# Optimization experiments

Hardware: AMD Instinct MI355X
Metric: run time of the kernel (lower is better)

## Reference

```python
import jax, jax.numpy as jnp
import numpy as np

NUM_CLASSES = 80
MAX_MATCHES = 10
ALPHA = 0.5
BETA = 6.0
EPS = 1e-9
IMG = 640.0


def _make_boxes(key, shape):
    # random valid xyxy boxes inside a 640x640 image
    k1, k2 = jax.random.split(key)
    c = jax.random.uniform(k1, shape + (2,)) * IMG
    wh = jax.random.uniform(k2, shape + (2,)) * (IMG * 0.3) + 4.0
    return jnp.concatenate([c - wh / 2, c + wh / 2], axis=-1).astype(jnp.float32)


def setup_inputs() -> dict:
    key = jax.random.key(0)
    ks = jax.random.split(key, 5)
    B, G = 32, 100
    # anchor center points for 640x640 input at strides 8/16/32 -> 8400 anchors
    pts = []
    for s in (8, 16, 32):
        n = 640 // s
        xs = (jnp.arange(n, dtype=jnp.float32) + 0.5) * s
        gy, gx = jnp.meshgrid(xs, xs, indexing="ij")
        pts.append(jnp.stack([gx.ravel(), gy.ravel()], axis=-1))
    anchors = jnp.concatenate(pts, axis=0)  # [8400, 2]
    A = anchors.shape[0]
    scores = jax.random.uniform(ks[0], (B, A, NUM_CLASSES), dtype=jnp.float32)
    decode_bboxes = _make_boxes(ks[1], (B, A))
    gt_bboxes = _make_boxes(ks[2], (B, G))
    gt_labels = jax.random.randint(ks[3], (B, G), 0, NUM_CLASSES, dtype=jnp.int32)
    gt_mask = jax.random.uniform(ks[4], (B, G)) < 0.8
    return {"scores": scores, "decode_bboxes": decode_bboxes, "anchors": anchors,
            "gt_labels": gt_labels, "gt_bboxes": gt_bboxes, "gt_mask": gt_mask}


def _pairwise_iou(gt, pred):
    # gt [B,G,4], pred [B,A,4] -> IoU [B,G,A]
    lt = jnp.maximum(gt[:, :, None, :2], pred[:, None, :, :2])
    rb = jnp.minimum(gt[:, :, None, 2:], pred[:, None, :, 2:])
    wh = jnp.clip(rb - lt, 0.0)
    inter = wh[..., 0] * wh[..., 1]
    area_g = (gt[..., 2] - gt[..., 0]) * (gt[..., 3] - gt[..., 1])
    area_p = (pred[..., 2] - pred[..., 0]) * (pred[..., 3] - pred[..., 1])
    return inter / (area_g[:, :, None] + area_p[:, None, :] - inter + EPS)


def _assign(scores, decode_bboxes, anchors, gt_labels, gt_bboxes, gt_mask):
    B, A, C = scores.shape
    G = gt_labels.shape[1]
    overlaps = _pairwise_iou(gt_bboxes, decode_bboxes)  # [B,G,A]
    # predicted score at each gt's class, per anchor -> [B,G,A]
    bbox_scores = jnp.take_along_axis(scores, gt_labels[:, None, :], axis=2)  # [B,A,G]
    bbox_scores = jnp.swapaxes(bbox_scores, 1, 2)  # [B,G,A]
    # task-aligned metric
    align = (bbox_scores ** ALPHA) * (overlaps ** BETA)
    # anchor center must lie inside the gt box
    ax = anchors[None, None, :, 0]
    ay = anchors[None, None, :, 1]
    in_box = ((ax > gt_bboxes[..., 0:1]) & (ax < gt_bboxes[..., 2:3]) &
              (ay > gt_bboxes[..., 1:2]) & (ay < gt_bboxes[..., 3:4]))
    align = jnp.where(gt_mask[:, :, None] & in_box, align, 0.0)
    # top-k candidate anchors per gt (scatter instead of one-hot to stay O(B*G*A))
    vals, idxs = jax.lax.top_k(align, MAX_MATCHES)  # [B,G,K]
    valid = (vals > 0).astype(align.dtype)
    bi = jnp.arange(B)[:, None, None]
    gi = jnp.arange(G)[None, :, None]
    matched = jnp.zeros((B, G, A), align.dtype).at[bi, gi, idxs].add(valid)  # [B,G,A] in {0,1}
    # resolve anchors matched to multiple gts: keep the gt with highest IoU
    overlaps_m = overlaps * matched
    gt_match = jnp.argmax(overlaps_m, axis=1)  # [B,A]
    fg = jnp.max(overlaps_m, axis=1) > 0  # [B,A]
    # gather box targets
    bbox_labels = jnp.take_along_axis(gt_bboxes, gt_match[:, :, None], axis=1)  # [B,A,4]
    bbox_labels = jnp.where(fg[:, :, None], bbox_labels, -1.0)
    # gather class targets
    cls = jnp.take_along_axis(gt_labels, gt_match, axis=1)  # [B,A]
    cls = jnp.where(fg, cls, -1)
    class_labels = jax.nn.one_hot(cls, C, dtype=scores.dtype)  # [B,A,C] (all-zero for -1)
    # normalize alignment metrics per gt, reduce to per-anchor scale
    align_m = align * matched
    max_align = jnp.max(align_m, axis=-1, keepdims=True)  # [B,G,1]
    max_ov = jnp.max(overlaps_m, axis=-1, keepdims=True)  # [B,G,1]
    norm = jnp.max(align_m * max_ov / (max_align + EPS), axis=1)  # [B,A]
    class_labels = class_labels * norm[..., None]
    return bbox_labels, class_labels, fg


def reference(scores, decode_bboxes, anchors, gt_labels, gt_bboxes, gt_mask):
    return _assign(scores, decode_bboxes, anchors, gt_labels, gt_bboxes, gt_mask)
```

## Files before the change

kernel.cpp:

```cpp
#include <hip/hip_runtime.h>

#define BB 32
#define AA 8400
#define GG 100
#define CC 80
#define KK 10
#define MAXC 1024

__global__ __launch_bounds__(256) void topk_assign(
    const float* __restrict__ scores,
    const float* __restrict__ dbox,
    const int*   __restrict__ gt_labels,
    const float* __restrict__ gt_bboxes,
    const int*   __restrict__ gt_mask,
    unsigned long long* __restrict__ packed,
    unsigned int* __restrict__ normb)
{
    const int bg = blockIdx.x;
    const int b = bg / GG;
    const int g = bg - b * GG;
    if (gt_mask[bg] == 0) return;

    const float4 gt = reinterpret_cast<const float4*>(gt_bboxes)[bg];
    const int label = gt_labels[bg];
    const int tid = threadIdx.x;

    int ix0_0, iy0_0, cx0, cy0, cnt0;
    int ix0_1, iy0_1, cx1, cy1, cnt1;
    int ix0_2, iy0_2, cx2, cy2, cnt2;
    {
        int xl = max((int)floorf(gt.x * 0.125f - 0.5f) + 1, 0);
        int xh = min((int)ceilf (gt.z * 0.125f - 0.5f) - 1, 79);
        int yl = max((int)floorf(gt.y * 0.125f - 0.5f) + 1, 0);
        int yh = min((int)ceilf (gt.w * 0.125f - 0.5f) - 1, 79);
        ix0_0 = xl; iy0_0 = yl;
        cx0 = max(xh - xl + 1, 0); cy0 = max(yh - yl + 1, 0);
        cnt0 = cx0 * cy0;
    }
    {
        int xl = max((int)floorf(gt.x * 0.0625f - 0.5f) + 1, 0);
        int xh = min((int)ceilf (gt.z * 0.0625f - 0.5f) - 1, 39);
        int yl = max((int)floorf(gt.y * 0.0625f - 0.5f) + 1, 0);
        int yh = min((int)ceilf (gt.w * 0.0625f - 0.5f) - 1, 39);
        ix0_1 = xl; iy0_1 = yl;
        cx1 = max(xh - xl + 1, 0); cy1 = max(yh - yl + 1, 0);
        cnt1 = cx1 * cy1;
    }
    {
        int xl = max((int)floorf(gt.x * 0.03125f - 0.5f) + 1, 0);
        int xh = min((int)ceilf (gt.z * 0.03125f - 0.5f) - 1, 19);
        int yl = max((int)floorf(gt.y * 0.03125f - 0.5f) + 1, 0);
        int yh = min((int)ceilf (gt.w * 0.03125f - 0.5f) - 1, 19);
        ix0_2 = xl; iy0_2 = yl;
        cx2 = max(xh - xl + 1, 0); cy2 = max(yh - yl + 1, 0);
        cnt2 = cx2 * cy2;
    }
    int total = cnt0 + cnt1 + cnt2;
    if (total > MAXC) total = MAXC;
    if (total == 0) return;

    __shared__ float c_align[MAXC];
    __shared__ float c_iou[MAXC];
    __shared__ int   c_a[MAXC];
    __shared__ float wv[KK], wov[KK];
    __shared__ int   wa[KK];
    __shared__ unsigned long long wred[4];
    __shared__ float s_stats[2];

    if (tid < KK) wv[tid] = 0.0f;

    const float area_g = (gt.z - gt.x) * (gt.w - gt.y);
    const float4* db = reinterpret_cast<const float4*>(dbox) + (size_t)b * AA;
    const float*  sc = scores + (size_t)b * AA * CC + label;

    for (int t = tid; t < total; t += 256) {
        int u = t, a;
        if (u < cnt0) {
            int ty = u / cx0; int tx = u - ty * cx0;
            a = (iy0_0 + ty) * 80 + (ix0_0 + tx);
        } else {
            u -= cnt0;
            if (u < cnt1) {
                int ty = u / cx1; int tx = u - ty * cx1;
                a = 6400 + (iy0_1 + ty) * 40 + (ix0_1 + tx);
            } else {
                u -= cnt1;
                int ty = u / cx2; int tx = u - ty * cx2;
                a = 8000 + (iy0_2 + ty) * 20 + (ix0_2 + tx);
            }
        }
        float4 p = db[a];
        float lx = fmaxf(gt.x, p.x), ly = fmaxf(gt.y, p.y);
        float rx = fminf(gt.z, p.z), ry = fminf(gt.w, p.w);
        float w = fmaxf(rx - lx, 0.0f), h = fmaxf(ry - ly, 0.0f);
        float inter = w * h;
        float area_p = (p.z - p.x) * (p.w - p.y);
        float iou = inter / (area_g + area_p - inter + 1e-9f);
        float s = sc[(size_t)a * CC];
        float i2 = iou * iou;
        c_align[t] = sqrtf(s) * (i2 * i2 * i2);
        c_iou[t]   = iou;
        c_a[t]     = a;
    }
    __syncthreads();

    for (int r = 0; r < KK; ++r) {
        float best = 0.0f; int bslot = -1;
        for (int i = tid; i < total; i += 256) {
            float v = c_align[i];
            if (v > best) { best = v; bslot = i; }
        }
        unsigned long long pk =
            ((unsigned long long)__float_as_uint(best) << 32) | (unsigned)bslot;
#pragma unroll
        for (int off = 32; off > 0; off >>= 1) {
            unsigned long long o = __shfl_xor(pk, off);
            if (o > pk) pk = o;
        }
        if ((tid & 63) == 0) wred[tid >> 6] = pk;
        __syncthreads();
        if (tid == 0) {
            unsigned long long m = wred[0];
            if (wred[1] > m) m = wred[1];
            if (wred[2] > m) m = wred[2];
            if (wred[3] > m) m = wred[3];
            float bv = __uint_as_float((unsigned)(m >> 32));
            int slot = (int)(unsigned)m;
            if (bv > 0.0f && slot >= 0) {
                wv[r] = bv; wov[r] = c_iou[slot]; wa[r] = c_a[slot];
                c_align[slot] = -1.0f;
            } else {
                wv[r] = 0.0f;
            }
        }
        __syncthreads();
        if (wv[r] <= 0.0f) break;
    }

    if (tid == 0) {
        float mo = 0.0f;
#pragma unroll
        for (int r = 0; r < KK; ++r)
            if (wv[r] > 0.0f) mo = fmaxf(mo, wov[r]);
        s_stats[0] = mo;
        s_stats[1] = wv[0];
    }
    __syncthreads();

    if (tid < KK && wv[tid] > 0.0f) {
        int a = wa[tid];
        float nval = wv[tid] * s_stats[0] / (s_stats[1] + 1e-9f);
        atomicMax(&normb[(size_t)b * AA + a], __float_as_uint(nval));
        unsigned long long pk =
            ((unsigned long long)__float_as_uint(wov[tid]) << 32) |
            (unsigned long long)(0xFFFFFFFFu - (unsigned)g);
        atomicMax(&packed[(size_t)b * AA + a], pk);
    }
}

__global__ __launch_bounds__(256) void finalize_anchor(
    const float* __restrict__ gt_bboxes,
    const int*   __restrict__ gt_labels,
    const unsigned long long* __restrict__ packed,
    float* __restrict__ out_bbox,
    float* __restrict__ out_fg,
    int*   __restrict__ cls_ws)
{
    int i = blockIdx.x * blockDim.x + threadIdx.x;
    if (i >= BB * AA) return;
    int b = i / AA;
    unsigned long long p = packed[i];
    bool fg = (p != 0ULL);
    float4 bb = make_float4(-1.0f, -1.0f, -1.0f, -1.0f);
    int cls = -1;
    if (fg) {
        int g = (int)(0xFFFFFFFFu - (unsigned)(p & 0xFFFFFFFFull));
        bb  = reinterpret_cast<const float4*>(gt_bboxes)[b * GG + g];
        cls = gt_labels[b * GG + g];
    }
    reinterpret_cast<float4*>(out_bbox)[i] = bb;
    out_fg[i] = fg ? 1.0f : 0.0f;
    cls_ws[i] = cls;
}

__global__ __launch_bounds__(256) void finalize_cls(
    const int* __restrict__ cls_ws,
    const unsigned int* __restrict__ normb,
    float4* __restrict__ out_cls4)
{
    int t = blockIdx.x * blockDim.x + threadIdx.x;
    if (t >= BB * AA * (CC / 4)) return;
    int ba = t / (CC / 4);
    int q  = t - ba * (CC / 4);
    int rel = cls_ws[ba] - q * 4;
    float4 v = make_float4(0.0f, 0.0f, 0.0f, 0.0f);
    if (rel >= 0 && rel < 4) {
        float nv = __uint_as_float(normb[ba]);
        if      (rel == 0) v.x = nv;
        else if (rel == 1) v.y = nv;
        else if (rel == 2) v.z = nv;
        else               v.w = nv;
    }
    out_cls4[t] = v;
}

extern "C" void kernel_launch(void* const* d_in, const int* in_sizes, int n_in,
                              void* d_out, int out_size, void* d_ws, size_t ws_size,
                              hipStream_t stream) {
    const float* scores    = (const float*)d_in[0];
    const float* dbox      = (const float*)d_in[1];
    const int*   gt_labels = (const int*)d_in[3];
    const float* gt_bboxes = (const float*)d_in[4];
    const int*   gt_mask   = (const int*)d_in[5];

    float* out = (float*)d_out;
    float* out_bbox = out;
    float* out_cls  = out + (size_t)BB * AA * 4;
    float* out_fg   = out + (size_t)BB * AA * (4 + CC);

    const size_t N = (size_t)BB * AA;
    unsigned long long* packed = (unsigned long long*)d_ws;
    unsigned int* normb = (unsigned int*)((char*)d_ws + N * 8);
    int* cls_ws = (int*)((char*)d_ws + N * 12);

    hipMemsetAsync(d_ws, 0, N * 12, stream);

    topk_assign<<<BB * GG, 256, 0, stream>>>(scores, dbox, gt_labels,
                                             gt_bboxes, gt_mask, packed, normb);
    finalize_anchor<<<(int)((N + 255) / 256), 256, 0, stream>>>(
        gt_bboxes, gt_labels, packed, out_bbox, out_fg, cls_ws);
    finalize_cls<<<(int)((N * (CC / 4) + 255) / 256), 256, 0, stream>>>(
        cls_ws, normb, (float4*)out_cls);
}
```

Before: 182.4 us.

## Use single-wavefront register top-k and fuse finalize kernels into one

```diff
diff --git a/kernel.cpp b/kernel.cpp
--- a/kernel.cpp
+++ b/kernel.cpp
@@ -25,17 +25,17 @@
     const int label = gt_labels[bg];
     const int tid = threadIdx.x;
 
-    int ix0_0, iy0_0, cx0, cy0, cnt0;
-    int ix0_1, iy0_1, cx1, cy1, cnt1;
-    int ix0_2, iy0_2, cx2, cy2, cnt2;
+    int ix0_0, iy0_0, cx0, cnt0;
+    int ix0_1, iy0_1, cx1, cnt1;
+    int ix0_2, iy0_2, cx2, cnt2;
     {
         int xl = max((int)floorf(gt.x * 0.125f - 0.5f) + 1, 0);
         int xh = min((int)ceilf (gt.z * 0.125f - 0.5f) - 1, 79);
         int yl = max((int)floorf(gt.y * 0.125f - 0.5f) + 1, 0);
         int yh = min((int)ceilf (gt.w * 0.125f - 0.5f) - 1, 79);
         ix0_0 = xl; iy0_0 = yl;
-        cx0 = max(xh - xl + 1, 0); cy0 = max(yh - yl + 1, 0);
-        cnt0 = cx0 * cy0;
+        cx0 = max(xh - xl + 1, 0);
+        cnt0 = cx0 * max(yh - yl + 1, 0);
     }
     {
         int xl = max((int)floorf(gt.x * 0.0625f - 0.5f) + 1, 0);
@@ -43,8 +43,8 @@
         int yl = max((int)floorf(gt.y * 0.0625f - 0.5f) + 1, 0);
         int yh = min((int)ceilf (gt.w * 0.0625f - 0.5f) - 1, 39);
         ix0_1 = xl; iy0_1 = yl;
-        cx1 = max(xh - xl + 1, 0); cy1 = max(yh - yl + 1, 0);
-        cnt1 = cx1 * cy1;
+        cx1 = max(xh - xl + 1, 0);
+        cnt1 = cx1 * max(yh - yl + 1, 0);
     }
     {
         int xl = max((int)floorf(gt.x * 0.03125f - 0.5f) + 1, 0);
@@ -52,8 +52,8 @@
         int yl = max((int)floorf(gt.y * 0.03125f - 0.5f) + 1, 0);
         int yh = min((int)ceilf (gt.w * 0.03125f - 0.5f) - 1, 19);
         ix0_2 = xl; iy0_2 = yl;
-        cx2 = max(xh - xl + 1, 0); cy2 = max(yh - yl + 1, 0);
-        cnt2 = cx2 * cy2;
+        cx2 = max(xh - xl + 1, 0);
+        cnt2 = cx2 * max(yh - yl + 1, 0);
     }
     int total = cnt0 + cnt1 + cnt2;
     if (total > MAXC) total = MAXC;
@@ -62,12 +62,6 @@
     __shared__ float c_align[MAXC];
     __shared__ float c_iou[MAXC];
     __shared__ int   c_a[MAXC];
-    __shared__ float wv[KK], wov[KK];
-    __shared__ int   wa[KK];
-    __shared__ unsigned long long wred[4];
-    __shared__ float s_stats[2];
-
-    if (tid < KK) wv[tid] = 0.0f;
 
     const float area_g = (gt.z - gt.x) * (gt.w - gt.y);
     const float4* db = reinterpret_cast<const float4*>(dbox) + (size_t)b * AA;
@@ -103,97 +97,84 @@
         c_a[t]     = a;
     }
     __syncthreads();
-
+    if (tid >= 64) return;
+
+    const int lane = tid;
+    float av[16];
+#pragma unroll
+    for (int i = 0; i < 16; ++i) {
+        int slot = lane + 64 * i;
+        av[i] = (slot < total) ? c_align[slot] : -1.0f;
+    }
+
+    unsigned used = 0;
+    float win_v = 0.0f;
+    int   win_slot = 0;
     for (int r = 0; r < KK; ++r) {
-        float best = 0.0f; int bslot = -1;
-        for (int i = tid; i < total; i += 256) {
-            float v = c_align[i];
-            if (v > best) { best = v; bslot = i; }
+        float best = 0.0f; int bi = 0; bool any = false;
+#pragma unroll
+        for (int i = 0; i < 16; ++i) {
+            bool ok = (((used >> i) & 1u) == 0u) && (av[i] > best);
+            best = ok ? av[i] : best;
+            bi   = ok ? i : bi;
+            any  = any || ok;
         }
+        unsigned slotenc = any ? (unsigned)(lane + (bi << 6)) : 0u;
         unsigned long long pk =
-            ((unsigned long long)__float_as_uint(best) << 32) | (unsigned)bslot;
+            ((unsigned long long)__float_as_uint(best) << 32) | slotenc;
 #pragma unroll
         for (int off = 32; off > 0; off >>= 1) {
             unsigned long long o = __shfl_xor(pk, off);
             if (o > pk) pk = o;
         }
-        if ((tid & 63) == 0) wred[tid >> 6] = pk;
-        __syncthreads();
-        if (tid == 0) {
-            unsigned long long m = wred[0];
-            if (wred[1] > m) m = wred[1];
-            if (wred[2] > m) m = wred[2];
-            if (wred[3] > m) m = wred[3];
-            float bv = __uint_as_float((unsigned)(m >> 32));
-            int slot = (int)(unsigned)m;
-            if (bv > 0.0f && slot >= 0) {
-                wv[r] = bv; wov[r] = c_iou[slot]; wa[r] = c_a[slot];
-                c_align[slot] = -1.0f;
-            } else {
-                wv[r] = 0.0f;
-            }
-        }
-        __syncthreads();
-        if (wv[r] <= 0.0f) break;
-    }
-
-    if (tid == 0) {
-        float mo = 0.0f;
-#pragma unroll
-        for (int r = 0; r < KK; ++r)
-            if (wv[r] > 0.0f) mo = fmaxf(mo, wov[r]);
-        s_stats[0] = mo;
-        s_stats[1] = wv[0];
-    }
-    __syncthreads();
-
-    if (tid < KK && wv[tid] > 0.0f) {
-        int a = wa[tid];
-        float nval = wv[tid] * s_stats[0] / (s_stats[1] + 1e-9f);
+        float bv = __uint_as_float((unsigned)(pk >> 32));
+        if (bv <= 0.0f) break;
+        int slot = (int)(pk & 0x3FFull);
+        if (lane == r) { win_v = bv; win_slot = slot; }
+        if (lane == (slot & 63)) used |= (1u << (slot >> 6));
+    }
+
+    bool valid = (lane < KK) && (win_v > 0.0f);
+    float myiou = valid ? c_iou[win_slot] : 0.0f;
+    float mo = myiou;
+#pragma unroll
+    for (int off = 32; off > 0; off >>= 1)
+        mo = fmaxf(mo, __shfl_xor(mo, off));
+    float ma = __shfl(win_v, 0);
+    if (valid) {
+        int a = c_a[win_slot];
+        float nval = win_v * mo / (ma + 1e-9f);
         atomicMax(&normb[(size_t)b * AA + a], __float_as_uint(nval));
-        unsigned long long pk =
-            ((unsigned long long)__float_as_uint(wov[tid]) << 32) |
+        unsigned long long pk2 =
+            ((unsigned long long)__float_as_uint(myiou) << 32) |
             (unsigned long long)(0xFFFFFFFFu - (unsigned)g);
-        atomicMax(&packed[(size_t)b * AA + a], pk);
+        atomicMax(&packed[(size_t)b * AA + a], pk2);
     }
 }
 
-__global__ __launch_bounds__(256) void finalize_anchor(
+__global__ __launch_bounds__(256) void finalize_all(
     const float* __restrict__ gt_bboxes,
     const int*   __restrict__ gt_labels,
     const unsigned long long* __restrict__ packed,
-    float* __restrict__ out_bbox,
-    float* __restrict__ out_fg,
-    int*   __restrict__ cls_ws)
-{
-    int i = blockIdx.x * blockDim.x + threadIdx.x;
-    if (i >= BB * AA) return;
-    int b = i / AA;
-    unsigned long long p = packed[i];
-    bool fg = (p != 0ULL);
-    float4 bb = make_float4(-1.0f, -1.0f, -1.0f, -1.0f);
-    int cls = -1;
-    if (fg) {
-        int g = (int)(0xFFFFFFFFu - (unsigned)(p & 0xFFFFFFFFull));
-        bb  = reinterpret_cast<const float4*>(gt_bboxes)[b * GG + g];
-        cls = gt_labels[b * GG + g];
-    }
-    reinterpret_cast<float4*>(out_bbox)[i] = bb;
-    out_fg[i] = fg ? 1.0f : 0.0f;
-    cls_ws[i] = cls;
-}
-
-__global__ __launch_bounds__(256) void finalize_cls(
-    const int* __restrict__ cls_ws,
     const unsigned int* __restrict__ normb,
-    float4* __restrict__ out_cls4)
+    float4* __restrict__ out_bbox4,
+    float4* __restrict__ out_cls4,
+    float*  __restrict__ out_fg)
 {
     int t = blockIdx.x * blockDim.x + threadIdx.x;
     if (t >= BB * AA * (CC / 4)) return;
     int ba = t / (CC / 4);
     int q  = t - ba * (CC / 4);
-    int rel = cls_ws[ba] - q * 4;
+    int b  = ba / AA;
+
+    unsigned long long p = packed[ba];
+    bool fg = (p != 0ULL);
+    int gidx = fg ? (b * GG + (int)(0xFFFFFFFFu - (unsigned)(p & 0xFFFFFFFFull)))
+                  : 0;
+    int cls = fg ? gt_labels[gidx] : -1;
+
     float4 v = make_float4(0.0f, 0.0f, 0.0f, 0.0f);
+    int rel = cls - q * 4;
     if (rel >= 0 && rel < 4) {
         float nv = __uint_as_float(normb[ba]);
         if      (rel == 0) v.x = nv;
@@ -202,6 +183,13 @@
         else               v.w = nv;
     }
     out_cls4[t] = v;
+
+    if (q == 0) {
+        float4 bb = fg ? reinterpret_cast<const float4*>(gt_bboxes)[gidx]
+                       : make_float4(-1.0f, -1.0f, -1.0f, -1.0f);
+        out_bbox4[ba] = bb;
+        out_fg[ba] = fg ? 1.0f : 0.0f;
+    }
 }
 
 extern "C" void kernel_launch(void* const* d_in, const int* in_sizes, int n_in,
@@ -221,14 +209,12 @@
     const size_t N = (size_t)BB * AA;
     unsigned long long* packed = (unsigned long long*)d_ws;
     unsigned int* normb = (unsigned int*)((char*)d_ws + N * 8);
-    int* cls_ws = (int*)((char*)d_ws + N * 12);
 
     hipMemsetAsync(d_ws, 0, N * 12, stream);
 
     topk_assign<<<BB * GG, 256, 0, stream>>>(scores, dbox, gt_labels,
                                              gt_bboxes, gt_mask, packed, normb);
-    finalize_anchor<<<(int)((N + 255) / 256), 256, 0, stream>>>(
-        gt_bboxes, gt_labels, packed, out_bbox, out_fg, cls_ws);
-    finalize_cls<<<(int)((N * (CC / 4) + 255) / 256), 256, 0, stream>>>(
-        cls_ws, normb, (float4*)out_cls);
+    finalize_all<<<(int)((N * (CC / 4) + 255) / 256), 256, 0, stream>>>(
+        gt_bboxes, gt_labels, packed, normb,
+        (float4*)out_bbox, (float4*)out_cls, out_fg);
 }
```

Result: no change. 179.7 us (-1.4%).
